# Optimization experiments

Measured on AMD Instinct MI355X. Metric: run time of the kernel, lower is better.

Reference implementation:

```python
import jax, jax.numpy as jnp
import numpy as np

NUM_SAMPLES = 5      # samples per line (line_matcher_cfg)
MIN_DIST_PTS = 8.0   # min pixel spacing between samples
TOP_K = 10           # top-k candidate lines for NW matching
GRID_SIZE = 4        # desc map stride
GAP = 0.1            # NW gap penalty


def sample_line_points(line_seg):
    # line_seg: (N, 2, 2) ij endpoints -> pts (N, S, 2), valid (N, S)
    start, end = line_seg[:, 0], line_seg[:, 1]
    lengths = jnp.linalg.norm(end - start, axis=1)
    nsamp = jnp.clip(jnp.floor(lengths / MIN_DIST_PTS), 2.0, float(NUM_SAMPLES))
    k = jnp.arange(NUM_SAMPLES, dtype=line_seg.dtype)
    interval = (end - start) / (nsamp - 1.0)[:, None]          # (N, 2)
    pts = start[:, None, :] + k[None, :, None] * interval[:, None, :]
    valid = k[None, :] < nsamp[:, None]
    pts = jnp.where(valid[..., None], pts, 0.0)                # torch pads with 0
    return pts, valid


def sample_descriptors(desc, pts):
    # Faithful F.grid_sample(bilinear, zeros padding, align_corners=False) after
    # kornia normalize_pixel_coordinates ((size-1) normalization), then L2-norm.
    # desc: (1, D, H, W); pts: (P, 2) ij coords in full-res image.
    D, H, W = desc.shape[1], desc.shape[2], desc.shape[3]
    img_h, img_w = H * GRID_SIZE, W * GRID_SIZE
    xn = 2.0 * pts[:, 1] / (img_w - 1) - 1.0
    yn = 2.0 * pts[:, 0] / (img_h - 1) - 1.0
    ix = ((xn + 1.0) * W - 1.0) / 2.0   # align_corners=False unnormalize
    iy = ((yn + 1.0) * H - 1.0) / 2.0
    x0f = jnp.floor(ix); y0f = jnp.floor(iy)
    wx = ix - x0f; wy = iy - y0f
    x0 = x0f.astype(jnp.int32); y0 = y0f.astype(jnp.int32)
    img = desc[0]

    def gather(xi, yi):
        inb = ((xi >= 0) & (xi < W) & (yi >= 0) & (yi < H)).astype(img.dtype)
        xc = jnp.clip(xi, 0, W - 1); yc = jnp.clip(yi, 0, H - 1)
        return img[:, yc, xc] * inb[None, :]   # (D, P), zeros outside

    v = (gather(x0, y0) * ((1 - wx) * (1 - wy))[None]
         + gather(x0 + 1, y0) * (wx * (1 - wy))[None]
         + gather(x0, y0 + 1) * ((1 - wx) * wy)[None]
         + gather(x0 + 1, y0 + 1) * (wx * wy)[None])
    return v / jnp.linalg.norm(v, axis=0, keepdims=True)


def needleman_wunsch(scores):
    # scores: (B, n, m); sequential DP via nested lax.scan (rows, then cols)
    B, n, m = scores.shape
    s = jnp.transpose(scores, (1, 0, 2)) - GAP  # (n, B, m)

    def row_step(prev_row, srow):               # prev_row (B, m+1), srow (B, m)
        diag = prev_row[:, :-1].T                # (m, B)
        up = prev_row[:, 1:].T                   # (m, B)

        def col_step(left, xs):
            d, u, sc = xs
            cur = jnp.maximum(jnp.maximum(left, u), d + sc)
            return cur, cur

        _, cols = jax.lax.scan(col_step, jnp.zeros((B,), s.dtype), (diag, up, srow.T))
        new_row = jnp.concatenate([jnp.zeros((B, 1), s.dtype), cols.T], axis=1)
        return new_row, None

    final, _ = jax.lax.scan(row_step, jnp.zeros((B, m + 1), s.dtype), s)
    return final[:, -1]


def filter_and_match_lines(scores):
    # scores: (N, M, n, n)
    ls1 = scores.max(3); v1 = (ls1 != -1.0).astype(scores.dtype)
    ls1 = (ls1 * v1).sum(2) / v1.sum(2)
    ls2 = scores.max(2); v2 = (ls2 != -1.0).astype(scores.dtype)
    ls2 = (ls2 * v2).sum(2) / v2.sum(2)
    line_scores = (ls1 + ls2) / 2.0
    topk_lines = jnp.argsort(line_scores, axis=1)[:, -TOP_K:]          # (N, k)
    top = jnp.take_along_axis(scores, topk_lines[:, :, None, None], axis=1)
    top = jnp.concatenate([top, jnp.flip(top, axis=-1)], axis=1)       # (N, 2k, n, n)
    N, top2k, n, m = top.shape
    nw = needleman_wunsch(top.reshape(N * top2k, n, m)).reshape(N, top2k)
    matches = jnp.argmax(nw, axis=1) % (top2k // 2)
    matches = topk_lines[jnp.arange(N), matches]
    return matches, nw


def match_forward(line_seg1, line_seg2, desc1, desc2):
    N, M = line_seg1.shape[0], line_seg2.shape[0]
    pts1, val1 = sample_line_points(line_seg1)
    pts2, val2 = sample_line_points(line_seg2)
    d1 = sample_descriptors(desc1, pts1.reshape(-1, 2))   # (D, N*S)
    d2 = sample_descriptors(desc2, pts2.reshape(-1, 2))   # (D, M*S)
    scores = d1.T @ d2                                    # (N*S, M*S)
    scores = jnp.where(val1.reshape(-1)[:, None], scores, -1.0)
    scores = jnp.where(val2.reshape(-1)[None, :], scores, -1.0)
    scores = scores.reshape(N, NUM_SAMPLES, M, NUM_SAMPLES).transpose(0, 2, 1, 3)
    matches, nw = filter_and_match_lines(scores)
    # cross check
    matches2, _ = filter_and_match_lines(scores.transpose(1, 0, 3, 2))
    mutual = matches2[matches] == jnp.arange(N)
    matches = jnp.where(mutual, matches, -1)
    return matches, nw


def setup_inputs():
    key = jax.random.key(0)
    k1, k2, k3, k4 = jax.random.split(key, 4)
    N = M = 1200; D = 128; H = W = 128
    img = float(H * GRID_SIZE - 1)
    line_seg1 = jax.random.uniform(k1, (N, 2, 2), jnp.float32) * img
    line_seg2 = jax.random.uniform(k2, (M, 2, 2), jnp.float32) * img
    desc1 = jax.random.normal(k3, (1, D, H, W), jnp.float32)
    desc2 = jax.random.normal(k4, (1, D, H, W), jnp.float32)
    return {"line_seg1": line_seg1, "line_seg2": line_seg2, "desc1": desc1, "desc2": desc2}


def reference(line_seg1, line_seg2, desc1, desc2):
    return match_forward(line_seg1, line_seg2, desc1, desc2)
```

## Files before the change

### kernel.cpp

```cpp
#include <hip/hip_runtime.h>
#include <hip/hip_bf16.h>


#define NLINES 1200
#define NS 5
#define DD 128
#define HH 128
#define WW 128
#define HW (HH*WW)
#define IMGM1 511.0f
#define GAPC 0.1f
#define NPAD 1216
#define PPAD (NPAD*NS)
#define KEXT 384
#define NCH (KEXT/32)
#define NGRP (PPAD/16)

typedef __attribute__((ext_vector_type(8))) short short8;
typedef __attribute__((ext_vector_type(4))) float f32x4;

__global__ void transpose_desc(const float* __restrict__ in1, float* __restrict__ out1,
                               const float* __restrict__ in2, float* __restrict__ out2) {
    const float* in = blockIdx.z ? in2 : in1;
    float* out = blockIdx.z ? out2 : out1;
    __shared__ float t[32][132];
    int s0 = blockIdx.x * 128;
    int d0 = blockIdx.y * 32;
    int tid = threadIdx.x;
    #pragma unroll
    for (int pass = 0; pass < 4; ++pass) {
        int idx = pass * 256 + tid;
        int dr = idx >> 5, si = idx & 31;
        float4 v = *(const float4*)&in[(size_t)(d0 + dr) * HW + s0 + 4 * si];
        *(float4*)&t[dr][4 * si] = v;
    }
    __syncthreads();
    #pragma unroll
    for (int pass = 0; pass < 4; ++pass) {
        int idx = pass * 256 + tid;
        int sr = idx >> 3, di = idx & 7;
        float4 v = { t[4 * di][sr], t[4 * di + 1][sr], t[4 * di + 2][sr], t[4 * di + 3][sr] };
        *(float4*)&out[(size_t)(s0 + sr) * DD + d0 + 4 * di] = v;
    }
}

__global__ void samplepack_kernel(const float* __restrict__ lseg1, const float* __restrict__ lseg2,
                                  const float* __restrict__ tdesc1, const float* __restrict__ tdesc2,
                                  const float* __restrict__ desc1, const float* __restrict__ desc2,
                                  short* __restrict__ Aext, short* __restrict__ Bext,
                                  float* __restrict__ val1, float* __restrict__ val2,
                                  int use_t) {
    int side = blockIdx.y;
    const float* lseg = side ? lseg2 : lseg1;
    const float* tdesc = side ? tdesc2 : tdesc1;
    const float* desc = side ? desc2 : desc1;
    short* Ef = side ? Bext : Aext;
    float* valout = side ? val2 : val1;
    int arole = side ? 0 : 1;

    __shared__ float ds[16][129];
    int g = blockIdx.x;
    int t = threadIdx.x;
    int lane = t & 63, w = t >> 6;

    #pragma unroll
    for (int s = 0; s < 4; ++s) {
        int r = w * 4 + s;
        int pt = g * 16 + r;
        int line = pt / NS;
        int k = pt - line * NS;

        float sy = 0.f, sx = 0.f, ey = 0.f, ex = 0.f;
        if (line < NLINES) {
            sy = lseg[line * 4 + 0]; sx = lseg[line * 4 + 1];
            ey = lseg[line * 4 + 2]; ex = lseg[line * 4 + 3];
        }
        float dy = ey - sy, dx = ex - sx;
        float len = sqrtf(dy * dy + dx * dx);
        float ns = floorf(len * 0.125f);
        ns = fminf(fmaxf(ns, 2.0f), 5.0f);
        float kf = (float)k;
        float validf = (kf < ns) ? 1.0f : 0.0f;
        float py = sy + kf * (dy / (ns - 1.0f));
        float px = sx + kf * (dx / (ns - 1.0f));
        if (validf == 0.0f) { py = 0.0f; px = 0.0f; }

        float xn = 2.0f * px / IMGM1 - 1.0f;
        float yn = 2.0f * py / IMGM1 - 1.0f;
        float ix = ((xn + 1.0f) * (float)WW - 1.0f) * 0.5f;
        float iy = ((yn + 1.0f) * (float)HH - 1.0f) * 0.5f;
        float x0f = floorf(ix), y0f = floorf(iy);
        float wx = ix - x0f, wy = iy - y0f;
        int x0 = (int)x0f, y0 = (int)y0f;

        float w00 = (1.0f - wx) * (1.0f - wy);
        float w10 = wx * (1.0f - wy);
        float w01 = (1.0f - wx) * wy;
        float w11 = wx * wy;

        float v0 = 0.0f, v1 = 0.0f;
        int xs[4] = { x0, x0 + 1, x0,     x0 + 1 };
        int ys[4] = { y0, y0,     y0 + 1, y0 + 1 };
        float ws4[4] = { w00, w10, w01, w11 };
        #pragma unroll
        for (int c = 0; c < 4; ++c) {
            int xi = xs[c], yi = ys[c];
            float inb = (xi >= 0 && xi < WW && yi >= 0 && yi < HH) ? 1.0f : 0.0f;
            int xc = min(max(xi, 0), WW - 1);
            int yc = min(max(yi, 0), HH - 1);
            if (use_t) {
                int base = (yc * WW + xc) * DD;
                v0 += tdesc[base + lane] * inb * ws4[c];
                v1 += tdesc[base + 64 + lane] * inb * ws4[c];
            } else {
                int base = yc * WW + xc;
                v0 += desc[lane * HW + base] * inb * ws4[c];
                v1 += desc[(lane + 64) * HW + base] * inb * ws4[c];
            }
        }
        float ss = v0 * v0 + v1 * v1;
        #pragma unroll
        for (int o = 32; o > 0; o >>= 1) ss += __shfl_xor(ss, o);
        if (ss == 0.0f) ss = 1.0f;
        float nrm = sqrtf(ss);
        ds[r][lane] = v0 / nrm;
        ds[r][64 + lane] = v1 / nrm;
        if (lane == 0) valout[pt] = (line < NLINES) ? validf : 0.0f;
    }
    __syncthreads();

    #pragma unroll
    for (int it = 0; it < 3; ++it) {
        int idx = it * 256 + t;
        int c = idx >> 6, l = idx & 63;
        int q = l >> 4, r = l & 15;
        short8 outv;
        #pragma unroll
        for (int jj = 0; jj < 8; ++jj) {
            int kext = c * 32 + q * 8 + jj;
            int term = kext >> 7, k = kext & 127;
            float x = ds[r][k];
            __hip_bfloat16 h = __float2bfloat16(x);
            short v = *(short*)&h;
            bool lo_term = arole ? (term == 1) : (term == 2);
            if (lo_term) {
                float hf = __bfloat162float(h);
                __hip_bfloat16 lw = __float2bfloat16(x - hf);
                v = *(short*)&lw;
            }
            outv[jj] = v;
        }
        *(short8*)&Ef[((size_t)(g * NCH + c) * 64 + l) * 8] = outv;
    }
}

__launch_bounds__(256, 2)
__global__ void score_kernel(const short* __restrict__ Af, const short* __restrict__ Bf,
                             const float* __restrict__ val1, const float* __restrict__ val2,
                             float* __restrict__ lsc, float* __restrict__ lscT) {
    __shared__ float dump[80 * 161];
    __shared__ float red[16][33];

    const int t = threadIdx.x;
    const int lane = t & 63;
    const int w = t >> 6;
    const int wm = w >> 1;
    const int wn = w & 1;
    const int gA0 = blockIdx.x * 10;
    const int gB0 = blockIdx.y * 10;

    const short* pa[5];
    const short* pb[5];
    #pragma unroll
    for (int ti = 0; ti < 5; ++ti) {
        pa[ti] = Af + ((size_t)(gA0 + 5 * wm + ti) * NCH * 64 + lane) * 8;
        pb[ti] = Bf + ((size_t)(gB0 + 5 * wn + ti) * NCH * 64 + lane) * 8;
    }

    f32x4 acc[5][5];
    #pragma unroll
    for (int a = 0; a < 5; ++a)
        #pragma unroll
        for (int b = 0; b < 5; ++b)
            acc[a][b] = (f32x4){0.f, 0.f, 0.f, 0.f};

    short8 ca[5], cb[5], na[5], nb[5];
    #pragma unroll
    for (int ti = 0; ti < 5; ++ti) {
        ca[ti] = *(const short8*)(pa[ti]);
        cb[ti] = *(const short8*)(pb[ti]);
    }
    #pragma unroll
    for (int c = 0; c < NCH; c += 2) {
        #pragma unroll
        for (int ti = 0; ti < 5; ++ti) {
            na[ti] = *(const short8*)(pa[ti] + (c + 1) * 512);
            nb[ti] = *(const short8*)(pb[ti] + (c + 1) * 512);
        }
        #pragma unroll
        for (int ti = 0; ti < 5; ++ti)
            #pragma unroll
            for (int tj = 0; tj < 5; ++tj)
                acc[ti][tj] = __builtin_amdgcn_mfma_f32_16x16x32_bf16(
                    ca[ti], cb[tj], acc[ti][tj], 0, 0, 0);
        if (c + 2 < NCH) {
            #pragma unroll
            for (int ti = 0; ti < 5; ++ti) {
                ca[ti] = *(const short8*)(pa[ti] + (c + 2) * 512);
                cb[ti] = *(const short8*)(pb[ti] + (c + 2) * 512);
            }
        }
        #pragma unroll
        for (int ti = 0; ti < 5; ++ti)
            #pragma unroll
            for (int tj = 0; tj < 5; ++tj)
                acc[ti][tj] = __builtin_amdgcn_mfma_f32_16x16x32_bf16(
                    na[ti], nb[tj], acc[ti][tj], 0, 0, 0);
    }

    const int i0l = blockIdx.x * 32;
    const int j0l = blockIdx.y * 32;
    #pragma unroll
    for (int p = 0; p < 2; ++p) {
        __syncthreads();
        if (wm == p) {
            #pragma unroll
            for (int ti = 0; ti < 5; ++ti) {
                #pragma unroll
                for (int reg = 0; reg < 4; ++reg) {
                    int rloc = 16 * ti + (lane >> 4) * 4 + reg;
                    #pragma unroll
                    for (int tj = 0; tj < 5; ++tj) {
                        int col = 80 * wn + 16 * tj + (lane & 15);
                        dump[rloc * 161 + col] = acc[ti][tj][reg];
                    }
                }
            }
        }
        __syncthreads();
        #pragma unroll
        for (int e = 0; e < 2; ++e) {
            int q = t * 2 + e;
            int li = q >> 5, lj = q & 31;
            int i = i0l + 16 * p + li;
            int j = j0l + lj;
            float S[5][5];
            #pragma unroll
            for (int a = 0; a < 5; ++a) {
                float va = val1[i * NS + a];
                #pragma unroll
                for (int b = 0; b < 5; ++b) {
                    float vb = val2[j * NS + b];
                    float sc = dump[(li * 5 + a) * 161 + (lj * 5 + b)];
                    S[a][b] = (va != 0.0f && vb != 0.0f) ? sc : -1.0f;
                }
            }
            float sum1 = 0.0f, cnt1 = 0.0f;
            #pragma unroll
            for (int a = 0; a < 5; ++a) {
                float r = S[a][0];
                #pragma unroll
                for (int b = 1; b < 5; ++b) r = fmaxf(r, S[a][b]);
                float v = (r != -1.0f) ? 1.0f : 0.0f;
                sum1 += r * v; cnt1 += v;
            }
            float sum2 = 0.0f, cnt2 = 0.0f;
            #pragma unroll
            for (int b = 0; b < 5; ++b) {
                float r = S[0][b];
                #pragma unroll
                for (int a = 1; a < 5; ++a) r = fmaxf(r, S[a][b]);
                float v = (r != -1.0f) ? 1.0f : 0.0f;
                sum2 += r * v; cnt2 += v;
            }
            float res = (sum1 / cnt1 + sum2 / cnt2) * 0.5f;
            red[li][lj] = res;
            if (i < NLINES && j < NLINES) lsc[i * NLINES + j] = res;
        }
        __syncthreads();
        #pragma unroll
        for (int e = 0; e < 2; ++e) {
            int q = t + 256 * e;
            int li = q & 15, lj = q >> 4;
            int i = i0l + 16 * p + li;
            int j = j0l + lj;
            if (i < NLINES && j < NLINES) lscT[j * NLINES + i] = red[li][lj];
        }
    }
}

__device__ __forceinline__ float nw5(const float* M) {
    float F[6] = {0, 0, 0, 0, 0, 0};
    #pragma unroll
    for (int x = 0; x < 5; ++x) {
        float diag = F[0];
        float left = 0.0f;
        #pragma unroll
        for (int y = 1; y <= 5; ++y) {
            float up = F[y];
            float cur = fmaxf(fmaxf(left, up), diag + (M[x * 5 + y - 1] - GAPC));
            F[y] = cur; left = cur; diag = up;
        }
    }
    return F[5];
}

__global__ void topk_nw_kernel(const float* __restrict__ lsc, const float* __restrict__ lscT,
                               const short* __restrict__ Af, const short* __restrict__ Bf,
                               const float* __restrict__ val1, const float* __restrict__ val2,
                               int* __restrict__ topk1, int* __restrict__ topk2,
                               float* __restrict__ nwout, float* __restrict__ nw2buf) {
    __shared__ short sh_lds[NCH * 512];
    __shared__ float sbuf[10][25];
    __shared__ int jl[10];
    __shared__ float wv[5];
    __shared__ int wi[5];
    int rb = blockIdx.x;
    int dir = (rb >= NLINES) ? 1 : 0;
    int row = rb - dir * NLINES;
    int t = threadIdx.x;
    int w = t >> 6;
    int lane = t & 63;
    int q = lane >> 4, rr = lane & 15;

    const short* shEf = dir ? Bf : Af;
    const short* cdEf = dir ? Af : Bf;
    const float* ls = dir ? (lscT + (size_t)row * NLINES) : (lsc + (size_t)row * NLINES);
    int* topk = dir ? (topk2 + row * 10) : (topk1 + row * 10);

    for (int idx = t; idx < NCH * 64; idx += 320) {
        int c = idx >> 6, l = idx & 63;
        int lq = l >> 4, lr = l & 15;
        int ptS = row * 5 + min(lr, 4);
        const short* gp = shEf + ((size_t)(ptS >> 4) * NCH * 64 + lq * 16 + (ptS & 15)) * 8
                               + (size_t)c * 512;
        *(short8*)&sh_lds[c * 512 + l * 8] = *(const short8*)gp;
    }

    float val[4];
    #pragma unroll
    for (int s = 0; s < 4; ++s) {
        int j = t + 320 * s;
        val[s] = (j < NLINES) ? ls[j] : -1e30f;
    }
    float bv = -1e30f; int bi = -1;
    #pragma unroll
    for (int s = 0; s < 4; ++s) {
        int j = t + 320 * s;
        if (val[s] >= bv) { bv = val[s]; bi = j; }
    }
    for (int sel = 0; sel < 10; ++sel) {
        float rv = bv; int ri = bi;
        #pragma unroll
        for (int o = 32; o > 0; o >>= 1) {
            float ov = __shfl_xor(rv, o);
            int oi = __shfl_xor(ri, o);
            if (ov > rv || (ov == rv && oi > ri)) { rv = ov; ri = oi; }
        }
        if (lane == 0) { wv[w] = rv; wi[w] = ri; }
        __syncthreads();
        float fv = wv[0]; int fi = wi[0];
        #pragma unroll
        for (int qq = 1; qq < 5; ++qq)
            if (wv[qq] > fv || (wv[qq] == fv && wi[qq] > fi)) { fv = wv[qq]; fi = wi[qq]; }
        if (t == 0) { topk[9 - sel] = fi; jl[9 - sel] = fi; }
        if (fi >= 0 && (fi % 320) == t) {
            val[fi / 320] = -1e30f;
            bv = -1e30f; bi = -1;
            #pragma unroll
            for (int s = 0; s < 4; ++s) {
                int j = t + 320 * s;
                if (val[s] >= bv) { bv = val[s]; bi = j; }
            }
        }
        __syncthreads();
    }

    int c1 = jl[2 * w], c2 = jl[2 * w + 1];
    int ptC = (rr < 8) ? (c1 * 5 + min(rr, 4)) : (c2 * 5 + min(rr - 8, 4));
    const short* cp = cdEf + ((size_t)(ptC >> 4) * NCH * 64 + q * 16 + (ptC & 15)) * 8;

    f32x4 acc = (f32x4){0.f, 0.f, 0.f, 0.f};
    #pragma unroll
    for (int c = 0; c < NCH; ++c) {
        short8 sh = *(const short8*)&sh_lds[c * 512 + lane * 8];
        short8 cb = *(const short8*)(cp + c * 512);
        acc = dir ? __builtin_amdgcn_mfma_f32_16x16x32_bf16(cb, sh, acc, 0, 0, 0)
                  : __builtin_amdgcn_mfma_f32_16x16x32_bf16(sh, cb, acc, 0, 0, 0);
    }
    #pragma unroll
    for (int reg = 0; reg < 4; ++reg) {
        int m = q * 4 + reg, n = rr;
        if (!dir) {
            if (m < 5 && n < 5) sbuf[2 * w][m * 5 + n] = acc[reg];
            if (m < 5 && n >= 8 && n < 13) sbuf[2 * w + 1][m * 5 + (n - 8)] = acc[reg];
        } else {
            if (m < 5 && n < 5) sbuf[2 * w][m * 5 + n] = acc[reg];
            if (m >= 8 && m < 13 && n < 5) sbuf[2 * w + 1][(m - 8) * 5 + n] = acc[reg];
        }
    }
    __syncthreads();

    if (t < 20) {
        int r = t >> 1, rev = t & 1;
        int i = dir ? jl[r] : row;
        int j = dir ? row : jl[r];
        float S[25];
        #pragma unroll
        for (int a = 0; a < 5; ++a) {
            float va = val1[i * NS + a];
            #pragma unroll
            for (int b = 0; b < 5; ++b) {
                float vb = val2[j * NS + b];
                S[a * 5 + b] = (va != 0.0f && vb != 0.0f) ? sbuf[r][a * 5 + b] : -1.0f;
            }
        }
        float M[25];
        #pragma unroll
        for (int x = 0; x < 5; ++x)
            #pragma unroll
            for (int y = 0; y < 5; ++y) {
                if (!dir) M[x * 5 + y] = rev ? S[x * 5 + (4 - y)] : S[x * 5 + y];
                else      M[x * 5 + y] = rev ? S[(4 - y) * 5 + x] : S[y * 5 + x];
            }
        float nwv = nw5(M);
        float* o = dir ? nw2buf : nwout;
        o[row * 20 + rev * 10 + r] = nwv;
    }
}

__global__ void argmax_final_kernel(const float* __restrict__ nw1, const float* __restrict__ nw2,
                                    const int* __restrict__ topk1, const int* __restrict__ topk2,
                                    float* __restrict__ out) {
    __shared__ int mpre[NLINES];
    __shared__ int m2[NLINES];
    int t = threadIdx.x;
    for (int qq = t; qq < 2 * NLINES; qq += 1024) {
        int dir = qq / NLINES, row = qq - dir * NLINES;
        const float* nw = (dir ? nw2 : nw1) + row * 20;
        float best = nw[0]; int bi = 0;
        #pragma unroll
        for (int q = 1; q < 20; ++q) {
            float v = nw[q];
            if (v > best) { best = v; bi = q; }
        }
        int m = (dir ? topk2 : topk1)[row * 10 + (bi % 10)];
        if (dir) m2[row] = m; else mpre[row] = m;
    }
    __syncthreads();
    for (int i = t; i < NLINES; i += 1024) {
        int m = mpre[i];
        out[i] = (m2[m] == i) ? (float)m : -1.0f;
    }
}

extern "C" void kernel_launch(void* const* d_in, const int* in_sizes, int n_in,
                              void* d_out, int out_size, void* d_ws, size_t ws_size,
                              hipStream_t stream) {
    const float* lseg1 = (const float*)d_in[0];
    const float* lseg2 = (const float*)d_in[1];
    const float* desc1 = (const float*)d_in[2];
    const float* desc2 = (const float*)d_in[3];
    float* out = (float*)d_out;

    float* wsf = (float*)d_ws;
    size_t off = 0;
    float* val1 = wsf + off;   off += PPAD;
    float* val2 = wsf + off;   off += PPAD;
    float* lsc = wsf + off;    off += (size_t)NLINES * NLINES;
    float* lscT = wsf + off;   off += (size_t)NLINES * NLINES;
    int* topk1 = (int*)(wsf + off); off += NLINES * 10;
    int* topk2 = (int*)(wsf + off); off += NLINES * 10;
    float* nw2buf = wsf + off; off += NLINES * 20;
    short* Aext = (short*)(wsf + off); off += (size_t)PPAD * KEXT / 2;
    short* Bext = (short*)(wsf + off); off += (size_t)PPAD * KEXT / 2;
    float* tdesc1 = wsf + off; off += (size_t)HW * DD;
    float* tdesc2 = wsf + off; off += (size_t)HW * DD;
    size_t need_full = off * sizeof(float);
    int use_t = (ws_size >= need_full) ? 1 : 0;

    if (use_t) {
        transpose_desc<<<dim3(HW / 128, DD / 32, 2), 256, 0, stream>>>(
            desc1, tdesc1, desc2, tdesc2);
    }
    samplepack_kernel<<<dim3(NGRP, 2), 256, 0, stream>>>(
        lseg1, lseg2, tdesc1, tdesc2, desc1, desc2, Aext, Bext, val1, val2, use_t);

    score_kernel<<<dim3(NPAD / 32, NPAD / 32), 256, 0, stream>>>(Aext, Bext, val1, val2,
                                                                 lsc, lscT);

    topk_nw_kernel<<<2 * NLINES, 320, 0, stream>>>(lsc, lscT, Aext, Bext, val1, val2,
                                                   topk1, topk2, out + NLINES, nw2buf);

    argmax_final_kernel<<<1, 1024, 0, stream>>>(out + NLINES, nw2buf, topk1, topk2, out);
}
```

Measured before the change: 182.9 us.

## Stage B operand tiles through LDS with async global-to-LDS copies

```diff
diff --git a/kernel.cpp b/kernel.cpp
--- a/kernel.cpp
+++ b/kernel.cpp
@@ -19,6 +19,12 @@
 typedef __attribute__((ext_vector_type(8))) short short8;
 typedef __attribute__((ext_vector_type(4))) float f32x4;
 
+__device__ __forceinline__ void async_cp16(const void* g, void* l) {
+    __builtin_amdgcn_global_load_lds(
+        (const __attribute__((address_space(1))) void*)g,
+        (__attribute__((address_space(3))) void*)l, 16, 0, 0);
+}
+
 __global__ void transpose_desc(const float* __restrict__ in1, float* __restrict__ out1,
                                const float* __restrict__ in2, float* __restrict__ out2) {
     const float* in = blockIdx.z ? in2 : in1;
@@ -158,8 +164,10 @@
 __global__ void score_kernel(const short* __restrict__ Af, const short* __restrict__ Bf,
                              const float* __restrict__ val1, const float* __restrict__ val2,
                              float* __restrict__ lsc, float* __restrict__ lscT) {
-    __shared__ float dump[80 * 161];
-    __shared__ float red[16][33];
+    __shared__ union {
+        struct { short B[2][5120]; } st;
+        struct { float dump[80 * 161]; float red[16][33]; } ep;
+    } u;
 
     const int t = threadIdx.x;
     const int lane = t & 63;
@@ -170,12 +178,9 @@
     const int gB0 = blockIdx.y * 10;
 
     const short* pa[5];
-    const short* pb[5];
-    #pragma unroll
-    for (int ti = 0; ti < 5; ++ti) {
+    #pragma unroll
+    for (int ti = 0; ti < 5; ++ti)
         pa[ti] = Af + ((size_t)(gA0 + 5 * wm + ti) * NCH * 64 + lane) * 8;
-        pb[ti] = Bf + ((size_t)(gB0 + 5 * wn + ti) * NCH * 64 + lane) * 8;
-    }
 
     f32x4 acc[5][5];
     #pragma unroll
@@ -184,38 +189,43 @@
         for (int b = 0; b < 5; ++b)
             acc[a][b] = (f32x4){0.f, 0.f, 0.f, 0.f};
 
-    short8 ca[5], cb[5], na[5], nb[5];
-    #pragma unroll
-    for (int ti = 0; ti < 5; ++ti) {
-        ca[ti] = *(const short8*)(pa[ti]);
-        cb[ti] = *(const short8*)(pb[ti]);
-    }
-    #pragma unroll
-    for (int c = 0; c < NCH; c += 2) {
-        #pragma unroll
-        for (int ti = 0; ti < 5; ++ti) {
-            na[ti] = *(const short8*)(pa[ti] + (c + 1) * 512);
-            nb[ti] = *(const short8*)(pb[ti] + (c + 1) * 512);
-        }
+    auto stageB = [&](int c, int b) {
+        if (w < 2) {
+            #pragma unroll
+            for (int p = 0; p < 5; ++p) {
+                int gi = w * 5 + p;
+                const short* g = Bf + ((size_t)((gB0 + gi) * NCH + c) * 64 + lane) * 8;
+                async_cp16(g, &u.st.B[b][gi * 512]);
+            }
+        }
+    };
+
+    short8 ca[5], na[5];
+    stageB(0, 0);
+    #pragma unroll
+    for (int ti = 0; ti < 5; ++ti) ca[ti] = *(const short8*)(pa[ti]);
+
+    #pragma unroll
+    for (int c = 0; c < NCH; ++c) {
+        __syncthreads();
+        if (c + 1 < NCH) {
+            stageB(c + 1, (c + 1) & 1);
+            #pragma unroll
+            for (int ti = 0; ti < 5; ++ti)
+                na[ti] = *(const short8*)(pa[ti] + (c + 1) * 512);
+        }
+        short8 bf_[5];
+        #pragma unroll
+        for (int tj = 0; tj < 5; ++tj)
+            bf_[tj] = *(const short8*)&u.st.B[c & 1][(5 * wn + tj) * 512 + lane * 8];
         #pragma unroll
         for (int ti = 0; ti < 5; ++ti)
             #pragma unroll
             for (int tj = 0; tj < 5; ++tj)
                 acc[ti][tj] = __builtin_amdgcn_mfma_f32_16x16x32_bf16(
-                    ca[ti], cb[tj], acc[ti][tj], 0, 0, 0);
-        if (c + 2 < NCH) {
-            #pragma unroll
-            for (int ti = 0; ti < 5; ++ti) {
-                ca[ti] = *(const short8*)(pa[ti] + (c + 2) * 512);
-                cb[ti] = *(const short8*)(pb[ti] + (c + 2) * 512);
-            }
-        }
-        #pragma unroll
-        for (int ti = 0; ti < 5; ++ti)
-            #pragma unroll
-            for (int tj = 0; tj < 5; ++tj)
-                acc[ti][tj] = __builtin_amdgcn_mfma_f32_16x16x32_bf16(
-                    na[ti], nb[tj], acc[ti][tj], 0, 0, 0);
+                    ca[ti], bf_[tj], acc[ti][tj], 0, 0, 0);
+        #pragma unroll
+        for (int ti = 0; ti < 5; ++ti) ca[ti] = na[ti];
     }
 
     const int i0l = blockIdx.x * 32;
@@ -232,7 +242,7 @@
                     #pragma unroll
                     for (int tj = 0; tj < 5; ++tj) {
                         int col = 80 * wn + 16 * tj + (lane & 15);
-                        dump[rloc * 161 + col] = acc[ti][tj][reg];
+                        u.ep.dump[rloc * 161 + col] = acc[ti][tj][reg];
                     }
                 }
             }
@@ -251,7 +261,7 @@
                 #pragma unroll
                 for (int b = 0; b < 5; ++b) {
                     float vb = val2[j * NS + b];
-                    float sc = dump[(li * 5 + a) * 161 + (lj * 5 + b)];
+                    float sc = u.ep.dump[(li * 5 + a) * 161 + (lj * 5 + b)];
                     S[a][b] = (va != 0.0f && vb != 0.0f) ? sc : -1.0f;
                 }
             }
@@ -274,7 +284,7 @@
                 sum2 += r * v; cnt2 += v;
             }
             float res = (sum1 / cnt1 + sum2 / cnt2) * 0.5f;
-            red[li][lj] = res;
+            u.ep.red[li][lj] = res;
             if (i < NLINES && j < NLINES) lsc[i * NLINES + j] = res;
         }
         __syncthreads();
@@ -284,7 +294,7 @@
             int li = q & 15, lj = q >> 4;
             int i = i0l + 16 * p + li;
             int j = j0l + lj;
-            if (i < NLINES && j < NLINES) lscT[j * NLINES + i] = red[li][lj];
+            if (i < NLINES && j < NLINES) lscT[j * NLINES + i] = u.ep.red[li][lj];
         }
     }
 }
```

Result: no change. 181.1 us (-1.0%).
